# Optimization experiments

Hardware: AMD Instinct MI355X
Metric: run time of the kernel (lower is better)

## Reference

```python
import jax, jax.numpy as jnp
import numpy as np

P = 8          # patch_size
DIM = 256      # embed dim
HEADS = 8
HEAD_DIM = DIM // HEADS
CH = 3
PATCH_DIM = CH * P * P  # 192
INNER = int(4.0 * DIM)  # 1024
SCALE = HEAD_DIM ** -0.5


def sine_pos_embedding(n, c, dtype=jnp.float32):
    # standard 1D sinusoidal position encoding, shape (n, c)
    pos = jnp.arange(n, dtype=jnp.float32)[:, None]            # (n,1)
    div = jnp.exp(jnp.arange(0, c, 2, dtype=jnp.float32) * (-np.log(10000.0) / c))
    pe = jnp.zeros((n, c), dtype=jnp.float32)
    pe = pe.at[:, 0::2].set(jnp.sin(pos * div))
    pe = pe.at[:, 1::2].set(jnp.cos(pos * div))
    return pe.astype(dtype)


def patchify(x):
    # (B,C,H,W) -> (B, n, p1*p2*C), matching 'b c (h p1) (w p2) -> b (h w) (p1 p2 c)'
    B, C, H, W = x.shape
    hp, wp = H // P, W // P
    x = x.reshape(B, C, hp, P, wp, P)
    x = x.transpose(0, 2, 4, 3, 5, 1)        # (B, hp, wp, p1, p2, C)
    return x.reshape(B, hp * wp, P * P * C)


def unpatchify(x, hp, wp):
    # (B, n, p1*p2*C) -> (B, C, H, W)
    B = x.shape[0]
    x = x.reshape(B, hp, wp, P, P, CH)
    x = x.transpose(0, 5, 1, 3, 2, 4)        # (B, C, hp, p1, wp, p2)
    return x.reshape(B, CH, hp * P, wp * P)


def setup_inputs() -> dict:
    key = jax.random.key(0)
    ks = jax.random.split(key, 16)
    B, H, W = 8, 256, 256
    s = 0.02
    img0 = jax.random.normal(ks[0], (B, CH, H, W), dtype=jnp.float32)
    img1 = jax.random.normal(ks[1], (B, CH, H, W), dtype=jnp.float32)
    mask = jax.random.randint(ks[2], (B, 1, H, W), 0, 2).astype(jnp.float32)
    return {
        "img0": img0,
        "img1": img1,
        "mask": mask,
        "w_patch": jax.random.normal(ks[3], (PATCH_DIM, DIM), jnp.float32) * s,
        "b_patch": jnp.zeros((DIM,), jnp.float32),
        "w_kv": jax.random.normal(ks[4], (DIM, 2 * DIM), jnp.float32) * s,
        "b_kv": jnp.zeros((2 * DIM,), jnp.float32),
        "w_qv": jax.random.normal(ks[5], (DIM, 2 * DIM), jnp.float32) * s,
        "b_qv": jnp.zeros((2 * DIM,), jnp.float32),
        "w_fc1": jax.random.normal(ks[6], (DIM, INNER), jnp.float32) * s,
        "b_fc1": jnp.zeros((INNER,), jnp.float32),
        "w_fc2": jax.random.normal(ks[7], (INNER, PATCH_DIM), jnp.float32) * s,
        "b_fc2": jnp.zeros((PATCH_DIM,), jnp.float32),
    }


def reference(img0, img1, mask, w_patch, b_patch, w_kv, b_kv, w_qv, b_qv,
              w_fc1, b_fc1, w_fc2, b_fc2):
    B, C, H, W = img0.shape
    hp, wp = H // P, W // P
    n = hp * wp

    x0 = patchify(img0) @ w_patch + b_patch   # (B, n, dim)
    x1 = patchify(img1) @ w_patch + b_patch
    pe = sine_pos_embedding(n, DIM)
    x0 = x0 + pe
    x1 = x1 + pe

    # img0 -> k, v
    kv = (x0 @ w_kv + b_kv).reshape(B, n, 2, HEADS, HEAD_DIM)
    kv = kv.transpose(2, 0, 3, 1, 4)          # (2, B, heads, n, hd)
    k, v = kv[0], kv[1]

    # img1 -> q (v1 unused in forward, matching torch code)
    qv = (x1 @ w_qv + b_qv).reshape(B, n, 2, DIM).transpose(2, 0, 1, 3)
    q = qv[0].reshape(B, n, HEADS, HEAD_DIM).transpose(0, 2, 1, 3)  # (B, heads, n, hd)

    dots = jnp.einsum('bhqd,bhkd->bhqk', q, k) * SCALE  # (B, heads, n, n)

    # mask: (B,1,H,W) -> per-patch sum -> binary -> additive bias over key dim
    msum = mask.reshape(B, 1, hp, P, wp, P).sum(axis=(3, 5)).reshape(B, 1, n)
    bias = jnp.where(msum > 0, 0.0, -100.0)[:, :, None, :]  # (B,1,1,n)

    attn = jax.nn.softmax(dots + bias, axis=-1)
    out = jnp.einsum('bhqk,bhkd->bhqd', attn, v)
    out = out.transpose(0, 2, 1, 3).reshape(B, n, DIM)

    # mlp2: Linear -> GELU(exact) -> Linear
    h = jax.nn.gelu(out @ w_fc1 + b_fc1, approximate=False)
    res = h @ w_fc2 + b_fc2                   # (B, n, patch_dim)

    return unpatchify(res, hp, wp)            # (B, C, H, W)
```

## Files before the change

### kernel.cpp

```cpp
#include <hip/hip_runtime.h>
#include <cstdint>
#include <cstddef>

typedef __bf16 bf16_t;
typedef uint32_t u32;
typedef __bf16 bf16x4 __attribute__((ext_vector_type(4)));
typedef __bf16 bf16x8 __attribute__((ext_vector_type(8)));
typedef float f32x4 __attribute__((ext_vector_type(4)));
typedef float f32x16 __attribute__((ext_vector_type(16)));

__device__ __forceinline__ void gload_lds16(const bf16_t* g, bf16_t* l) {
  __builtin_amdgcn_global_load_lds((const __attribute__((address_space(1))) void*)g,
                                   (__attribute__((address_space(3))) void*)l,
                                   16, 0, 0);
}

__device__ __forceinline__ f32x4 mfma16(bf16x8 a, bf16x8 b, f32x4 c) {
  return __builtin_amdgcn_mfma_f32_16x16x32_bf16(a, b, c, 0, 0, 0);
}
__device__ __forceinline__ f32x16 mfma32(bf16x8 a, bf16x8 b, f32x16 c) {
  return __builtin_amdgcn_mfma_f32_32x32x16_bf16(a, b, c, 0, 0, 0);
}

#define LOG2E 1.4426950408889634f

__global__ __launch_bounds__(256)
void prep_all(const float* __restrict__ img0, const float* __restrict__ img1,
              const float* __restrict__ mask,
              const float* __restrict__ wp, const float* __restrict__ wkv,
              const float* __restrict__ wqv, const float* __restrict__ wfc1,
              const float* __restrict__ wfc2,
              bf16_t* __restrict__ xp0, bf16_t* __restrict__ xp1,
              float* __restrict__ pe, float* __restrict__ bias,
              bf16_t* __restrict__ wpT, bf16_t* __restrict__ wkvT,
              bf16_t* __restrict__ wqT, bf16_t* __restrict__ wfc1T,
              bf16_t* __restrict__ wfc2T) {
  __shared__ float tl[64 * 65];
  int bid = blockIdx.x, tid = threadIdx.x;
  if (bid < 1536) {
    int imgsel = bid >= 768;
    int t = (bid - (imgsel ? 768 : 0)) * 256 + tid;
    const float* img = imgsel ? img1 : img0;
    bf16_t* xp = imgsel ? xp1 : xp0;
    int wpp = t & 31, p1 = (t >> 5) & 7, hp = (t >> 8) & 31, rest = t >> 13;
    int b = rest / 3, c = rest - b * 3;
    const float* src = img + (((size_t)(b * 3 + c) * 256 + hp * 8 + p1) * 256 + wpp * 8);
    float4 v0 = *(const float4*)src;
    float4 v1 = *(const float4*)(src + 4);
    int row = b * 1024 + hp * 32 + wpp;
    bf16_t* dst = xp + (size_t)row * 192 + p1 * 24 + c;
    dst[0]  = (bf16_t)v0.x; dst[3]  = (bf16_t)v0.y; dst[6]  = (bf16_t)v0.z; dst[9]  = (bf16_t)v0.w;
    dst[12] = (bf16_t)v1.x; dst[15] = (bf16_t)v1.y; dst[18] = (bf16_t)v1.z; dst[21] = (bf16_t)v1.w;
  } else if (bid < 2560) {
    int t = bid - 1536, c = tid;
    int i2 = c & ~1;
    float div = __expf((float)i2 * (-9.210340371976184f / 256.0f));
    float arg = (float)t * div;
    float sv, cv;
    __sincosf(arg, &sv, &cv);
    pe[t * 256 + c] = (c & 1) ? cv : sv;
  } else if (bid < 2592) {
    int g = (bid - 2560) * 256 + tid;
    int b = g >> 10, t = g & 1023, hp = t >> 5, wpp = t & 31;
    const float* mp = mask + ((size_t)b * 256 + hp * 8) * 256 + wpp * 8;
    float s = 0.f;
    #pragma unroll
    for (int p1 = 0; p1 < 8; p1++) {
      float4 a = *(const float4*)(mp + p1 * 256);
      float4 c = *(const float4*)(mp + p1 * 256 + 4);
      s += a.x + a.y + a.z + a.w + c.x + c.y + c.z + c.w;
    }
    bias[g] = (s > 0.f) ? 0.f : (-100.f * LOG2E);
  } else {
    int i = bid - 2592;
    const float* src; bf16_t* dst; int srcN, dstK, NT;
    if (i >= 172) {
      int j = i - 172;
      bf16_t* p = wfc2T + 192 * 1024 + j * 8192 + tid * 32;
      bf16x8 z;
      #pragma unroll
      for (int e = 0; e < 8; e++) z[e] = (bf16_t)0.0f;
      *(bf16x8*)(p) = z; *(bf16x8*)(p + 8) = z;
      *(bf16x8*)(p + 16) = z; *(bf16x8*)(p + 24) = z;
      return;
    }
    if (i < 12)       { src = wp;   dst = wpT;   srcN = 256;  dstK = 192;  NT = 4; }
    else if (i < 44)  { i -= 12;  src = wkv;  dst = wkvT;  srcN = 512;  dstK = 256;  NT = 8; }
    else if (i < 60)  { i -= 44;  src = wqv;  dst = wqT;   srcN = 512;  dstK = 256;  NT = 4; }
    else if (i < 124) { i -= 60;  src = wfc1; dst = wfc1T; srcN = 1024; dstK = 256;  NT = 16; }
    else              { i -= 124; src = wfc2; dst = wfc2T; srcN = 192;  dstK = 1024; NT = 3; }
    int kt = i / NT, nt = i - kt * NT;
    #pragma unroll
    for (int j = 0; j < 4; j++) {
      int r = (tid >> 4) + 16 * j, c = (tid & 15) * 4;
      float4 v = *(const float4*)(src + (size_t)(kt * 64 + r) * srcN + nt * 64 + c);
      tl[r * 65 + c] = v.x; tl[r * 65 + c + 1] = v.y;
      tl[r * 65 + c + 2] = v.z; tl[r * 65 + c + 3] = v.w;
    }
    __syncthreads();
    #pragma unroll
    for (int j = 0; j < 16; j++) {
      int flat = tid + 256 * j;
      int n_l = flat >> 6, k_l = flat & 63;
      dst[(size_t)(nt * 64 + n_l) * dstK + kt * 64 + k_l] = (bf16_t)tl[k_l * 65 + n_l];
    }
  }
}

template<int EPI, int BN>
__global__ __launch_bounds__(256)
void gemm_bt(const bf16_t* __restrict__ A_, const bf16_t* __restrict__ A2,
             const bf16_t* __restrict__ Bt_, const bf16_t* __restrict__ Bt2,
             int M, int N, int K,
             const float* __restrict__ bias_, const float* __restrict__ bias2,
             const float* __restrict__ pe,
             bf16_t* __restrict__ out_b, bf16_t* __restrict__ out_b2,
             bf16_t* __restrict__ out_b3, float* __restrict__ out_f) {
  constexpr int NF = BN / 32;
  __shared__ bf16_t alds[2][8 * 64 * 8];
  __shared__ bf16_t blds[2][8 * BN * 8];
  const int tid = threadIdx.x;
  const int lane = tid & 63, wid = tid >> 6;
  const int ln15 = lane & 15, hi = lane >> 4;
  const int brow = blockIdx.x * 64;
  int bcol = blockIdx.y * BN;
  const bf16_t* A = A_;
  const bf16_t* Bt = Bt_;
  const float* bias = bias_;
  bool qpart = false;
  if (EPI == 0 && blockIdx.z) A = A2;
  if (EPI == 5 && blockIdx.y >= 4) {
    qpart = true; A = A2; Bt = Bt2; bias = bias2; bcol -= 512;
  }
  const int wr = wid >> 1, wc = wid & 1;

  auto stage = [&](int buf, int k0) {
    #pragma unroll
    for (int s = 0; s < 2; s++) {
      int c = tid + s * 256; int kb = c >> 6, row = c & 63;
      gload_lds16(A + (size_t)(brow + row) * K + k0 + kb * 8,
                  &alds[buf][(size_t)(s * 256 + wid * 64) * 8]);
    }
    #pragma unroll
    for (int s = 0; s < BN / 32; s++) {
      int c = tid + s * 256; int kb = c / BN, row = c & (BN - 1);
      gload_lds16(Bt + (size_t)(bcol + row) * K + k0 + kb * 8,
                  &blds[buf][(size_t)(s * 256 + wid * 64) * 8]);
    }
  };

  f32x4 acc[2][NF];
  #pragma unroll
  for (int m = 0; m < 2; m++)
    #pragma unroll
    for (int n = 0; n < NF; n++) acc[m][n] = (f32x4){0.f, 0.f, 0.f, 0.f};

  stage(0, 0);
  __syncthreads();
  int cur = 0;
  const int NT = K >> 6;
  for (int t = 0; t < NT; t++) {
    if (t + 1 < NT) stage(cur ^ 1, (t + 1) << 6);
    bf16x8 af[2][2], bfr[2][NF];
    #pragma unroll
    for (int kk = 0; kk < 2; kk++) {
      #pragma unroll
      for (int m = 0; m < 2; m++)
        af[kk][m] = *(const bf16x8*)&alds[cur][(size_t)((kk * 4 + hi) * 64 + wr * 32 + m * 16 + ln15) * 8];
      #pragma unroll
      for (int n = 0; n < NF; n++)
        bfr[kk][n] = *(const bf16x8*)&blds[cur][(size_t)((kk * 4 + hi) * BN + wc * (BN / 2) + n * 16 + ln15) * 8];
    }
    #pragma unroll
    for (int kk = 0; kk < 2; kk++)
      #pragma unroll
      for (int m = 0; m < 2; m++)
        #pragma unroll
        for (int n = 0; n < NF; n++)
          acc[m][n] = mfma16(af[kk][m], bfr[kk][n], acc[m][n]);
    __syncthreads();
    cur ^= 1;
  }

  #pragma unroll
  for (int m = 0; m < 2; m++) {
    #pragma unroll
    for (int n = 0; n < NF; n++) {
      #pragma unroll
      for (int r = 0; r < 4; r++) {
        int grow = brow + wr * 32 + m * 16 + hi * 4 + r;
        int gcol = bcol + wc * (BN / 2) + n * 16 + ln15;
        float v = acc[m][n][r];
        if (EPI == 0) {
          v += bias[gcol] + pe[(grow & 1023) * 256 + gcol];
          bf16_t* outx = blockIdx.z ? out_b2 : out_b;
          outx[(size_t)grow * N + gcol] = (bf16_t)v;
        } else if (EPI == 5) {
          v += bias[gcol];
          int b = grow >> 10, t = grow & 1023;
          if (!qpart) {
            if (gcol < 256) {
              int h = gcol >> 5, d = gcol & 31;
              out_b[(((size_t)(b * 8 + h) * 1024 + t) << 5) + d] = (bf16_t)v;
            } else {
              int c2 = gcol - 256; int h = c2 >> 5, d = c2 & 31;
              out_b2[(((size_t)(b * 8 + h) * 32 + d) << 10) + t] = (bf16_t)v;
            }
          } else {
            v *= (0.17677669529663687f * LOG2E);
            int h = gcol >> 5, d = gcol & 31;
            out_b3[(((size_t)(b * 8 + h) * 1024 + t) << 5) + d] = (bf16_t)v;
          }
        } else if (EPI == 3) {
          v += bias[gcol];
          float gg = 0.5f * v * (1.0f + erff(v * 0.7071067811865476f));
          out_b[(size_t)grow * N + gcol] = (bf16_t)gg;
        } else if (EPI == 4) {
          if (gcol < 192) {
            v += bias[gcol];
            int b = grow >> 10, t = grow & 1023;
            int hp = t >> 5, wpp = t & 31;
            int p = gcol / 3; int c = gcol - p * 3;
            int p1 = p >> 3, p2 = p & 7;
            out_f[(((size_t)(b * 3 + c) * 256 + hp * 8 + p1) * 256) + wpp * 8 + p2] = v;
          }
        }
      }
    }
  }
}

union PW { u32 w[4]; bf16x8 v; };

__device__ __forceinline__ u32 pkbf(float a, float b) {
  union { bf16_t h[2]; u32 w; } u;
  u.h[0] = (bf16_t)a; u.h[1] = (bf16_t)b;
  return u.w;
}

__device__ __forceinline__ void pl32swap(u32& a, u32& b) {
  asm volatile("v_permlane32_swap_b32 %0, %1" : "+v"(a), "+v"(b));
}

__device__ __forceinline__ void stage_kvb(const bf16_t* kbase, const bf16_t* vbase,
                                          const float* bb, int ch,
                                          bf16_t* kl, bf16_t* vl, float* blp,
                                          int tid, int wid, int lane) {
  #pragma unroll
  for (int p = 0; p < 4; p++) {
    int s = p * 256 + tid;
    int row = s >> 2, cs = (s & 3) ^ (row & 3);
    const bf16_t* src = kbase + (size_t)(ch * 256 + row) * 32 + cs * 8;
    gload_lds16(src, kl + (size_t)(p * 256 + wid * 64) * 8);
  }
  #pragma unroll
  for (int p = 0; p < 4; p++) {
    int s = p * 256 + tid;
    int row = s >> 5, cs = (s & 31) ^ row;
    const bf16_t* src = vbase + (size_t)row * 1024 + ch * 256 + cs * 8;
    gload_lds16(src, vl + (size_t)(p * 256 + wid * 64) * 8);
  }
  if (wid == 0)
    gload_lds16((const bf16_t*)(bb + ch * 256) + lane * 8, (bf16_t*)blp);
}

__global__ __launch_bounds__(256, 2)
void attn_kernel(const bf16_t* __restrict__ q, const bf16_t* __restrict__ k,
                 const bf16_t* __restrict__ vt, const float* __restrict__ bias,
                 bf16_t* __restrict__ out) {
  __shared__ bf16_t klds[2][1024 * 8];
  __shared__ bf16_t vlds[2][1024 * 8];
  __shared__ float bl[2][256];
  __shared__ float LSL[4][32];
  int tid = threadIdx.x, lane = tid & 63, wid = tid >> 6;
  int l31 = lane & 31, g = lane >> 5;
  int x = blockIdx.x & 7, idx = blockIdx.x >> 3;
  int qt = idx & 7;
  int bh = ((idx >> 3) << 3) | x;
  int b = bh >> 3, h = bh & 7;
  int q0 = qt * 128 + wid * 32;
  const bf16_t* qp = q + ((size_t)bh * 1024 + q0 + l31) * 32;
  bf16x8 qf0 = *(const bf16x8*)(qp + g * 8);
  bf16x8 qf1 = *(const bf16x8*)(qp + 16 + g * 8);
  const bf16_t* kbase = k + (size_t)bh * 32768;
  const bf16_t* vbase = vt + (size_t)bh * 32768;
  const float* bb = bias + b * 1024;

  f32x16 acc;
  #pragma unroll
  for (int r = 0; r < 16; r++) acc[r] = 0.f;
  float lsum = 0.f;

  stage_kvb(kbase, vbase, bb, 0, klds[0], vlds[0], bl[0], tid, wid, lane);
  __syncthreads();

  int cur = 0;
  for (int ch = 0; ch < 4; ch++) {
    if (ch < 3) stage_kvb(kbase, vbase, bb, ch + 1, klds[cur ^ 1], vlds[cur ^ 1], bl[cur ^ 1], tid, wid, lane);
    const bf16_t* kl = klds[cur];
    const bf16_t* vl = vlds[cur];
    const float* bp = bl[cur];
    #pragma unroll
    for (int kt = 0; kt < 8; kt++) {
      int row0 = kt * 32 + l31;
      bf16x8 kA = *(const bf16x8*)(kl + (size_t)(row0 * 4 + (g ^ (row0 & 3))) * 8);
      bf16x8 kB = *(const bf16x8*)(kl + (size_t)(row0 * 4 + ((2 + g) ^ (row0 & 3))) * 8);
      bf16x8 vA = *(const bf16x8*)(vl + (size_t)(l31 * 32 + ((4 * kt + g) ^ l31)) * 8);
      bf16x8 vB = *(const bf16x8*)(vl + (size_t)(l31 * 32 + ((4 * kt + 2 + g) ^ l31)) * 8);
      f32x4 c0 = *(const f32x4*)&bp[kt * 32 + 4 * g];
      f32x4 c1 = *(const f32x4*)&bp[kt * 32 + 8 + 4 * g];
      f32x4 c2 = *(const f32x4*)&bp[kt * 32 + 16 + 4 * g];
      f32x4 c3 = *(const f32x4*)&bp[kt * 32 + 24 + 4 * g];
      f32x16 S;
      S[0] = c0[0]; S[1] = c0[1]; S[2] = c0[2]; S[3] = c0[3];
      S[4] = c1[0]; S[5] = c1[1]; S[6] = c1[2]; S[7] = c1[3];
      S[8] = c2[0]; S[9] = c2[1]; S[10] = c2[2]; S[11] = c2[3];
      S[12] = c3[0]; S[13] = c3[1]; S[14] = c3[2]; S[15] = c3[3];
      S = mfma32(kA, qf0, S);
      S = mfma32(kB, qf1, S);
      float p[16];
      #pragma unroll
      for (int r = 0; r < 16; r++) p[r] = exp2f(S[r]);
      lsum += (((p[0] + p[1]) + (p[2] + p[3])) + ((p[4] + p[5]) + (p[6] + p[7]))) +
              (((p[8] + p[9]) + (p[10] + p[11])) + ((p[12] + p[13]) + (p[14] + p[15])));
      u32 w[8];
      #pragma unroll
      for (int j = 0; j < 8; j++) w[j] = pkbf(p[2 * j], p[2 * j + 1]);
      u32 xa = w[2], ya = w[0]; pl32swap(xa, ya);
      u32 xb = w[3], yb = w[1]; pl32swap(xb, yb);
      u32 xc = w[6], yc = w[4]; pl32swap(xc, yc);
      u32 xd = w[7], yd = w[5]; pl32swap(xd, yd);
      PW A0, A1;
      A0.w[0] = g ? xa : w[0];  A0.w[2] = g ? w[2] : ya;
      A0.w[1] = g ? xb : w[1];  A0.w[3] = g ? w[3] : yb;
      A1.w[0] = g ? xc : w[4];  A1.w[2] = g ? w[6] : yc;
      A1.w[1] = g ? xd : w[5];  A1.w[3] = g ? w[7] : yd;
      acc = mfma32(A0.v, vA, acc);
      acc = mfma32(A1.v, vB, acc);
    }
    __syncthreads();
    cur ^= 1;
  }

  lsum += __shfl_xor(lsum, 32);
  LSL[wid][l31] = lsum;
  #pragma unroll
  for (int r = 0; r < 16; r++) {
    int row = (r & 3) + 8 * (r >> 2) + 4 * g;
    float linv = 1.f / LSL[wid][row];
    out[((size_t)b * 1024 + q0 + row) * 256 + h * 32 + l31] = (bf16_t)(acc[r] * linv);
  }
}

extern "C" void kernel_launch(void* const* d_in, const int* in_sizes, int n_in,
                              void* d_out, int out_size, void* d_ws, size_t ws_size,
                              hipStream_t stream) {
  (void)in_sizes; (void)n_in; (void)out_size; (void)ws_size;
  const float* img0    = (const float*)d_in[0];
  const float* img1    = (const float*)d_in[1];
  const float* mask    = (const float*)d_in[2];
  const float* w_patch = (const float*)d_in[3];
  const float* b_patch = (const float*)d_in[4];
  const float* w_kv    = (const float*)d_in[5];
  const float* b_kv    = (const float*)d_in[6];
  const float* w_qv    = (const float*)d_in[7];
  const float* b_qv    = (const float*)d_in[8];
  const float* w_fc1   = (const float*)d_in[9];
  const float* b_fc1   = (const float*)d_in[10];
  const float* w_fc2   = (const float*)d_in[11];
  const float* b_fc2   = (const float*)d_in[12];
  float* out = (float*)d_out;

  char* ws = (char*)d_ws;
  float*  pe    = (float*)(ws + 0);
  float*  bias  = (float*)(ws + 1048576);
  bf16_t* wpT   = (bf16_t*)(ws + 1081344);
  bf16_t* wkvT  = (bf16_t*)(ws + 1179648);
  bf16_t* wqT   = (bf16_t*)(ws + 1441792);
  bf16_t* wfc1T = (bf16_t*)(ws + 1572864);
  bf16_t* wfc2T = (bf16_t*)(ws + 2097152);
  bf16_t* xp0   = (bf16_t*)(ws + 2621440);
  bf16_t* xp1   = (bf16_t*)(ws + 5767168);
  bf16_t* x0    = (bf16_t*)(ws + 8912896);
  bf16_t* x1    = (bf16_t*)(ws + 13107200);
  bf16_t* kbuf  = (bf16_t*)(ws + 17301504);
  bf16_t* vtbuf = (bf16_t*)(ws + 21495808);
  bf16_t* qbuf  = (bf16_t*)(ws + 25690112);
  bf16_t* aout  = (bf16_t*)(ws + 29884416);
  bf16_t* hbuf  = (bf16_t*)(ws + 34078720);

  prep_all<<<2772, 256, 0, stream>>>(img0, img1, mask, w_patch, w_kv, w_qv, w_fc1, w_fc2,
                                     xp0, xp1, pe, bias, wpT, wkvT, wqT, wfc1T, wfc2T);

  gemm_bt<0, 128><<<dim3(128, 2, 2), 256, 0, stream>>>(xp0, xp1, wpT, nullptr, 8192, 256, 192,
                                                       b_patch, nullptr, pe, x0, x1, nullptr, nullptr);
  gemm_bt<5, 128><<<dim3(128, 6), 256, 0, stream>>>(x0, x1, wkvT, wqT, 8192, 512, 256,
                                                    b_kv, b_qv, nullptr, kbuf, vtbuf, qbuf, nullptr);

  attn_kernel<<<512, 256, 0, stream>>>(qbuf, kbuf, vtbuf, bias, aout);
  attn_kernel<<<512, 256, 0, stream>>>(qbuf, kbuf, vtbuf, bias, aout);

  gemm_bt<3, 128><<<dim3(128, 8), 256, 0, stream>>>(aout, nullptr, wfc1T, nullptr, 8192, 1024, 256,
                                                    b_fc1, nullptr, nullptr, hbuf, nullptr, nullptr, nullptr);
  gemm_bt<4, 64><<<dim3(128, 4), 256, 0, stream>>>(hbuf, nullptr, wfc2T, nullptr, 8192, 256, 1024,
                                                   b_fc2, nullptr, nullptr, nullptr, nullptr, nullptr, out);
}
```

Before: 143.2 us.

## Split attention keys across waves and drop the duplicate attention launch

The attention kernel now gives each block 32 queries and has the four waves split the key dimension, each wave handling 32 keys per 128-key chunk. Partial outputs and row sums are then combined through shared memory in a final reduction. This creates 2048 smaller blocks with less LDS each and allows higher occupancy (launch bounds 4); the bias is read straight from global memory instead of being staged. It also removes a redundant second launch of the attention kernel, at the cost of an extra LDS reduction and sync at the end of each block.

```diff
diff --git a/kernel.cpp b/kernel.cpp
--- a/kernel.cpp
+++ b/kernel.cpp
@@ -242,43 +242,42 @@
   asm volatile("v_permlane32_swap_b32 %0, %1" : "+v"(a), "+v"(b));
 }
 
-__device__ __forceinline__ void stage_kvb(const bf16_t* kbase, const bf16_t* vbase,
-                                          const float* bb, int ch,
-                                          bf16_t* kl, bf16_t* vl, float* blp,
-                                          int tid, int wid, int lane) {
-  #pragma unroll
-  for (int p = 0; p < 4; p++) {
-    int s = p * 256 + tid;
-    int row = s >> 2, cs = (s & 3) ^ (row & 3);
-    const bf16_t* src = kbase + (size_t)(ch * 256 + row) * 32 + cs * 8;
-    gload_lds16(src, kl + (size_t)(p * 256 + wid * 64) * 8);
-  }
-  #pragma unroll
-  for (int p = 0; p < 4; p++) {
-    int s = p * 256 + tid;
-    int row = s >> 5, cs = (s & 31) ^ row;
-    const bf16_t* src = vbase + (size_t)row * 1024 + ch * 256 + cs * 8;
-    gload_lds16(src, vl + (size_t)(p * 256 + wid * 64) * 8);
-  }
-  if (wid == 0)
-    gload_lds16((const bf16_t*)(bb + ch * 256) + lane * 8, (bf16_t*)blp);
-}
-
-__global__ __launch_bounds__(256, 2)
+#define SMEM_BYTES 32768
+
+__device__ __forceinline__ void stage_kv(const bf16_t* kbase, const bf16_t* vbase,
+                                         int ch, char* smem, int cur,
+                                         int tid, int wid) {
+  bf16_t* kl = (bf16_t*)(smem + cur * 8192);
+  bf16_t* vl = (bf16_t*)(smem + 16384 + cur * 8192);
+  #pragma unroll
+  for (int s = 0; s < 2; s++) {
+    int c = tid + s * 256;
+    int row = c >> 2, cs = (c & 3) ^ (row & 3);
+    gload_lds16(kbase + (size_t)(ch * 128 + row) * 32 + cs * 8,
+                kl + (size_t)(s * 256 + wid * 64) * 8);
+  }
+  #pragma unroll
+  for (int s = 0; s < 2; s++) {
+    int c = tid + s * 256;
+    int row = c >> 4, cs = (c & 15) ^ (row & 15);
+    gload_lds16(vbase + (size_t)row * 1024 + ch * 128 + cs * 8,
+                vl + (size_t)(s * 256 + wid * 64) * 8);
+  }
+}
+
+__global__ __launch_bounds__(256, 4)
 void attn_kernel(const bf16_t* __restrict__ q, const bf16_t* __restrict__ k,
                  const bf16_t* __restrict__ vt, const float* __restrict__ bias,
                  bf16_t* __restrict__ out) {
-  __shared__ bf16_t klds[2][1024 * 8];
-  __shared__ bf16_t vlds[2][1024 * 8];
-  __shared__ float bl[2][256];
-  __shared__ float LSL[4][32];
+  __shared__ __align__(16) char smem[SMEM_BYTES];
+
   int tid = threadIdx.x, lane = tid & 63, wid = tid >> 6;
   int l31 = lane & 31, g = lane >> 5;
   int x = blockIdx.x & 7, idx = blockIdx.x >> 3;
-  int qt = idx & 7;
-  int bh = ((idx >> 3) << 3) | x;
+  int qt = idx & 31;
+  int bh = ((idx >> 5) << 3) | x;
   int b = bh >> 3, h = bh & 7;
-  int q0 = qt * 128 + wid * 32;
+  int q0 = qt * 32;
   const bf16_t* qp = q + ((size_t)bh * 1024 + q0 + l31) * 32;
   bf16x8 qf0 = *(const bf16x8*)(qp + g * 8);
   bf16x8 qf1 = *(const bf16x8*)(qp + 16 + g * 8);
@@ -291,65 +290,78 @@
   for (int r = 0; r < 16; r++) acc[r] = 0.f;
   float lsum = 0.f;
 
-  stage_kvb(kbase, vbase, bb, 0, klds[0], vlds[0], bl[0], tid, wid, lane);
+  stage_kv(kbase, vbase, 0, smem, 0, tid, wid);
   __syncthreads();
 
   int cur = 0;
-  for (int ch = 0; ch < 4; ch++) {
-    if (ch < 3) stage_kvb(kbase, vbase, bb, ch + 1, klds[cur ^ 1], vlds[cur ^ 1], bl[cur ^ 1], tid, wid, lane);
-    const bf16_t* kl = klds[cur];
-    const bf16_t* vl = vlds[cur];
-    const float* bp = bl[cur];
-    #pragma unroll
-    for (int kt = 0; kt < 8; kt++) {
-      int row0 = kt * 32 + l31;
-      bf16x8 kA = *(const bf16x8*)(kl + (size_t)(row0 * 4 + (g ^ (row0 & 3))) * 8);
-      bf16x8 kB = *(const bf16x8*)(kl + (size_t)(row0 * 4 + ((2 + g) ^ (row0 & 3))) * 8);
-      bf16x8 vA = *(const bf16x8*)(vl + (size_t)(l31 * 32 + ((4 * kt + g) ^ l31)) * 8);
-      bf16x8 vB = *(const bf16x8*)(vl + (size_t)(l31 * 32 + ((4 * kt + 2 + g) ^ l31)) * 8);
-      f32x4 c0 = *(const f32x4*)&bp[kt * 32 + 4 * g];
-      f32x4 c1 = *(const f32x4*)&bp[kt * 32 + 8 + 4 * g];
-      f32x4 c2 = *(const f32x4*)&bp[kt * 32 + 16 + 4 * g];
-      f32x4 c3 = *(const f32x4*)&bp[kt * 32 + 24 + 4 * g];
-      f32x16 S;
-      S[0] = c0[0]; S[1] = c0[1]; S[2] = c0[2]; S[3] = c0[3];
-      S[4] = c1[0]; S[5] = c1[1]; S[6] = c1[2]; S[7] = c1[3];
-      S[8] = c2[0]; S[9] = c2[1]; S[10] = c2[2]; S[11] = c2[3];
-      S[12] = c3[0]; S[13] = c3[1]; S[14] = c3[2]; S[15] = c3[3];
-      S = mfma32(kA, qf0, S);
-      S = mfma32(kB, qf1, S);
-      float p[16];
-      #pragma unroll
-      for (int r = 0; r < 16; r++) p[r] = exp2f(S[r]);
-      lsum += (((p[0] + p[1]) + (p[2] + p[3])) + ((p[4] + p[5]) + (p[6] + p[7]))) +
-              (((p[8] + p[9]) + (p[10] + p[11])) + ((p[12] + p[13]) + (p[14] + p[15])));
-      u32 w[8];
-      #pragma unroll
-      for (int j = 0; j < 8; j++) w[j] = pkbf(p[2 * j], p[2 * j + 1]);
-      u32 xa = w[2], ya = w[0]; pl32swap(xa, ya);
-      u32 xb = w[3], yb = w[1]; pl32swap(xb, yb);
-      u32 xc = w[6], yc = w[4]; pl32swap(xc, yc);
-      u32 xd = w[7], yd = w[5]; pl32swap(xd, yd);
-      PW A0, A1;
-      A0.w[0] = g ? xa : w[0];  A0.w[2] = g ? w[2] : ya;
-      A0.w[1] = g ? xb : w[1];  A0.w[3] = g ? w[3] : yb;
-      A1.w[0] = g ? xc : w[4];  A1.w[2] = g ? w[6] : yc;
-      A1.w[1] = g ? xd : w[5];  A1.w[3] = g ? w[7] : yd;
-      acc = mfma32(A0.v, vA, acc);
-      acc = mfma32(A1.v, vB, acc);
-    }
+  for (int ch = 0; ch < 8; ch++) {
+    if (ch < 7) stage_kv(kbase, vbase, ch + 1, smem, cur ^ 1, tid, wid);
+    const bf16_t* kl = (const bf16_t*)(smem + cur * 8192);
+    const bf16_t* vl = (const bf16_t*)(smem + 16384 + cur * 8192);
+    int base = ch * 128 + wid * 32;
+    int row0 = wid * 32 + l31;
+    bf16x8 kA = *(const bf16x8*)(kl + (size_t)(row0 * 4 + (g ^ (row0 & 3))) * 8);
+    bf16x8 kB = *(const bf16x8*)(kl + (size_t)(row0 * 4 + ((2 + g) ^ (row0 & 3))) * 8);
+    bf16x8 vA = *(const bf16x8*)(vl + (size_t)(l31 * 16 + ((wid * 4 + g) ^ (l31 & 15))) * 8);
+    bf16x8 vB = *(const bf16x8*)(vl + (size_t)(l31 * 16 + ((wid * 4 + 2 + g) ^ (l31 & 15))) * 8);
+    f32x4 c0 = *(const f32x4*)(bb + base + 4 * g);
+    f32x4 c1 = *(const f32x4*)(bb + base + 8 + 4 * g);
+    f32x4 c2 = *(const f32x4*)(bb + base + 16 + 4 * g);
+    f32x4 c3 = *(const f32x4*)(bb + base + 24 + 4 * g);
+    f32x16 S;
+    S[0] = c0[0]; S[1] = c0[1]; S[2] = c0[2]; S[3] = c0[3];
+    S[4] = c1[0]; S[5] = c1[1]; S[6] = c1[2]; S[7] = c1[3];
+    S[8] = c2[0]; S[9] = c2[1]; S[10] = c2[2]; S[11] = c2[3];
+    S[12] = c3[0]; S[13] = c3[1]; S[14] = c3[2]; S[15] = c3[3];
+    S = mfma32(kA, qf0, S);
+    S = mfma32(kB, qf1, S);
+    float p[16];
+    #pragma unroll
+    for (int r = 0; r < 16; r++) p[r] = exp2f(S[r]);
+    lsum += (((p[0] + p[1]) + (p[2] + p[3])) + ((p[4] + p[5]) + (p[6] + p[7]))) +
+            (((p[8] + p[9]) + (p[10] + p[11])) + ((p[12] + p[13]) + (p[14] + p[15])));
+    u32 w[8];
+    #pragma unroll
+    for (int j = 0; j < 8; j++) w[j] = pkbf(p[2 * j], p[2 * j + 1]);
+    u32 xa = w[2], ya = w[0]; pl32swap(xa, ya);
+    u32 xb = w[3], yb = w[1]; pl32swap(xb, yb);
+    u32 xc = w[6], yc = w[4]; pl32swap(xc, yc);
+    u32 xd = w[7], yd = w[5]; pl32swap(xd, yd);
+    PW A0, A1;
+    A0.w[0] = g ? xa : w[0];  A0.w[2] = g ? w[2] : ya;
+    A0.w[1] = g ? xb : w[1];  A0.w[3] = g ? w[3] : yb;
+    A1.w[0] = g ? xc : w[4];  A1.w[2] = g ? w[6] : yc;
+    A1.w[1] = g ? xd : w[5];  A1.w[3] = g ? w[7] : yd;
+    acc = mfma32(A0.v, vA, acc);
+    acc = mfma32(A1.v, vB, acc);
     __syncthreads();
     cur ^= 1;
   }
 
-  lsum += __shfl_xor(lsum, 32);
-  LSL[wid][l31] = lsum;
+  float* OL = (float*)smem;
+  float* LS = (float*)(smem + 16896);
   #pragma unroll
   for (int r = 0; r < 16; r++) {
     int row = (r & 3) + 8 * (r >> 2) + 4 * g;
-    float linv = 1.f / LSL[wid][row];
-    out[((size_t)b * 1024 + q0 + row) * 256 + h * 32 + l31] = (bf16_t)(acc[r] * linv);
-  }
+    OL[wid * 1056 + row * 33 + l31] = acc[r];
+  }
+  lsum += __shfl_xor(lsum, 32);
+  LS[wid * 32 + l31] = lsum;
+  __syncthreads();
+
+  int qq = tid >> 3, d0 = (tid & 7) * 4;
+  float l = LS[qq] + LS[32 + qq] + LS[64 + qq] + LS[96 + qq];
+  float o0 = 0.f, o1 = 0.f, o2 = 0.f, o3 = 0.f;
+  #pragma unroll
+  for (int w2 = 0; w2 < 4; w2++) {
+    const float* p = &OL[w2 * 1056 + qq * 33 + d0];
+    o0 += p[0]; o1 += p[1]; o2 += p[2]; o3 += p[3];
+  }
+  float linv = 1.f / l;
+  bf16x4 ov;
+  ov[0] = (bf16_t)(o0 * linv); ov[1] = (bf16_t)(o1 * linv);
+  ov[2] = (bf16_t)(o2 * linv); ov[3] = (bf16_t)(o3 * linv);
+  *(bf16x4*)(out + ((size_t)b * 1024 + q0 + qq) * 256 + h * 32 + d0) = ov;
 }
 
 extern "C" void kernel_launch(void* const* d_in, const int* in_sizes, int n_in,
@@ -397,8 +409,7 @@
   gemm_bt<5, 128><<<dim3(128, 6), 256, 0, stream>>>(x0, x1, wkvT, wqT, 8192, 512, 256,
                                                     b_kv, b_qv, nullptr, kbuf, vtbuf, qbuf, nullptr);
 
-  attn_kernel<<<512, 256, 0, stream>>>(qbuf, kbuf, vtbuf, bias, aout);
-  attn_kernel<<<512, 256, 0, stream>>>(qbuf, kbuf, vtbuf, bias, aout);
+  attn_kernel<<<2048, 256, 0, stream>>>(qbuf, kbuf, vtbuf, bias, aout);
 
   gemm_bt<3, 128><<<dim3(128, 8), 256, 0, stream>>>(aout, nullptr, wfc1T, nullptr, 8192, 1024, 256,
                                                     b_fc1, nullptr, nullptr, hbuf, nullptr, nullptr, nullptr);
```

Result: faster. 117.7 us (-17.8%).
